# Performance work log

Hardware: AMD Instinct MI355X
Metric: run time of the kernel (lower is better)

The kernel has to match this reference:

```python
import jax, jax.numpy as jnp
import numpy as np

B, N, E, H = 16, 1024, 128, 8  # batch, num_patches, emb_dim, num_heads
INNER = E * H                   # inner_dim = emb_dim * num_heads = 1024
LN_EPS = 1e-5
NEG_MAX = jnp.finfo(jnp.float32).max  # module uses -finfo.max on the diagonal


def setup_inputs() -> dict:
    key = jax.random.key(0)
    k0, k1, k2 = jax.random.split(key, 3)
    x = jax.random.normal(k0, (B, N, E), dtype=jnp.float32)
    ln_w = jnp.ones((E,), jnp.float32)
    ln_b = jnp.zeros((E,), jnp.float32)
    w_qkv = jax.random.normal(k1, (E, 3 * INNER), jnp.float32) * (E ** -0.5)
    scale = jnp.full((H,), E ** -0.5, jnp.float32)  # learnable per-head LSA scale
    w_proj = jax.random.normal(k2, (INNER, E), jnp.float32) * (INNER ** -0.5)
    b_proj = jnp.zeros((E,), jnp.float32)
    return {"x": x, "ln_w": ln_w, "ln_b": ln_b, "w_qkv": w_qkv,
            "scale": scale, "w_proj": w_proj, "b_proj": b_proj}


def reference(x, ln_w, ln_b, w_qkv, scale, w_proj, b_proj):
    # LayerNorm over emb_dim
    mu = jnp.mean(x, axis=-1, keepdims=True)
    var = jnp.mean(jnp.square(x - mu), axis=-1, keepdims=True)
    xn = (x - mu) * jax.lax.rsqrt(var + LN_EPS) * ln_w + ln_b

    # QKV projection (no bias), chunk into q,k,v of [B,N,INNER]
    qkv = xn @ w_qkv
    q, k, v = jnp.split(qkv, 3, axis=-1)

    # 'b n (h d) -> b h n d' with h = H, d = E
    def to_heads(t):
        return t.reshape(B, N, H, E).transpose(0, 2, 1, 3)
    q, k, v = to_heads(q), to_heads(k), to_heads(v)

    # per-head learnable scale (LSA), then mask diagonal to -max
    dots = jnp.einsum("bhnd,bhmd->bhnm", q, k) * scale[None, :, None, None]
    idx = jnp.arange(N)
    dots = dots.at[:, :, idx, idx].set(-NEG_MAX)

    attn = jax.nn.softmax(dots, axis=-1)  # dropout p=0.0 -> identity
    out = jnp.einsum("bhnm,bhmd->bhnd", attn, v)

    # 'b h n d -> b n (h d)', then output projection (with bias)
    out = out.transpose(0, 2, 1, 3).reshape(B, N, INNER)
    return out @ w_proj + b_proj
```

## Files before the change

### kernel.cpp

```cpp
#include <hip/hip_runtime.h>
#include <hip/hip_bf16.h>

typedef __bf16 bf16x8 __attribute__((ext_vector_type(8)));
typedef _Float16 f16x4 __attribute__((ext_vector_type(4)));
typedef float f32x4 __attribute__((ext_vector_type(4)));

__device__ __forceinline__ unsigned short f2bf(float f) {
  union { __hip_bfloat16 h; unsigned short u; } cv;
  cv.h = __float2bfloat16(f);
  return cv.u;
}
__device__ __forceinline__ unsigned short f2h(float f) {
  union { _Float16 h; unsigned short u; } cv;
  cv.h = (_Float16)f;
  return cv.u;
}

__device__ __forceinline__ bf16x8 ld_frag(const unsigned short* p) {
  bf16x8 v;
  __builtin_memcpy(&v, __builtin_assume_aligned(p, 16), 16);
  return v;
}
__device__ __forceinline__ f16x4 ld_h4(const unsigned short* p) {
  f16x4 v;
  __builtin_memcpy(&v, __builtin_assume_aligned(p, 8), 8);
  return v;
}
__device__ __forceinline__ uint4 ld16(const unsigned short* p) {
  uint4 v;
  __builtin_memcpy(&v, __builtin_assume_aligned(p, 16), 16);
  return v;
}
__device__ __forceinline__ void st16(unsigned short* p, uint4 v) {
  __builtin_memcpy(__builtin_assume_aligned(p, 16), &v, 16);
}
__device__ __forceinline__ void dma16(const unsigned short* g, unsigned short* l) {
  __builtin_amdgcn_global_load_lds((const __attribute__((address_space(1))) void*)g,
                                   (__attribute__((address_space(3))) void*)l, 16, 0, 0);
}

__global__ __launch_bounds__(256) void ln_kernel(const float* __restrict__ x,
                                                 const float* __restrict__ w,
                                                 const float* __restrict__ b,
                                                 unsigned short* __restrict__ xn) {
  int wave = threadIdx.x >> 6;
  int lane = threadIdx.x & 63;
  int row = blockIdx.x * 4 + wave;
  const float* xr = x + (size_t)row * 128;
  float2 v = *reinterpret_cast<const float2*>(xr + lane * 2);
  float s1 = v.x + v.y;
  float s2 = v.x * v.x + v.y * v.y;
#pragma unroll
  for (int off = 32; off > 0; off >>= 1) {
    s1 += __shfl_xor(s1, off, 64);
    s2 += __shfl_xor(s2, off, 64);
  }
  float mu = s1 * (1.0f / 128.0f);
  float var = s2 * (1.0f / 128.0f) - mu * mu;
  float rstd = rsqrtf(var + 1e-5f);
  float a0 = (v.x - mu) * rstd * w[lane * 2] + b[lane * 2];
  float a1 = (v.y - mu) * rstd * w[lane * 2 + 1] + b[lane * 2 + 1];
  unsigned int pk = (unsigned int)f2bf(a0) | ((unsigned int)f2bf(a1) << 16);
  *reinterpret_cast<unsigned int*>(xn + (size_t)row * 128 + lane * 2) = pk;
}

__global__ __launch_bounds__(256) void tcast_kernel(const float* __restrict__ in,
                                                    unsigned short* __restrict__ out,
                                                    int R, int C) {
  __shared__ float tile[32][33];
  int tx = threadIdx.x & 31, ty = threadIdx.x >> 5;
  int c0 = blockIdx.x * 32, r0 = blockIdx.y * 32;
#pragma unroll
  for (int k = 0; k < 4; k++)
    tile[ty + 8 * k][tx] = in[(size_t)(r0 + ty + 8 * k) * C + c0 + tx];
  __syncthreads();
#pragma unroll
  for (int k = 0; k < 4; k++)
    out[(size_t)(c0 + ty + 8 * k) * R + r0 + tx] = f2bf(tile[tx][ty + 8 * k]);
}

__global__ __launch_bounds__(256) void qkv_gemm(const unsigned short* __restrict__ A,
                                                const unsigned short* __restrict__ Bt,
                                                const float* __restrict__ scale,
                                                unsigned short* __restrict__ qk,
                                                unsigned short* __restrict__ Vt) {
  __shared__ unsigned short Al[128 * 72];
  __shared__ unsigned short Bl[128 * 72];
  int t = threadIdx.x;
  int i0 = blockIdx.x * 128, c0 = blockIdx.y * 128;
  int lg = t & 7, rr = t >> 3;
  int w = t >> 6, lane = t & 63, l15 = lane & 15, quad = lane >> 4;
  int wy = (w >> 1) * 64, wx = (w & 1) * 64;
  const f32x4 fz = {0.f, 0.f, 0.f, 0.f};
  f32x4 acc[4][4];
#pragma unroll
  for (int i = 0; i < 4; i++)
#pragma unroll
    for (int j = 0; j < 4; j++) acc[i][j] = fz;

#pragma unroll
  for (int kt = 0; kt < 2; kt++) {
    int k0 = kt * 64;
    uint4 areg[4], breg[4];
#pragma unroll
    for (int p = 0; p < 4; p++)
      areg[p] = ld16(&A[(size_t)(i0 + rr + 32 * p) * 128 + k0 + lg * 8]);
#pragma unroll
    for (int p = 0; p < 4; p++)
      breg[p] = ld16(&Bt[(size_t)(c0 + rr + 32 * p) * 128 + k0 + lg * 8]);
    __syncthreads();
#pragma unroll
    for (int p = 0; p < 4; p++) st16(&Al[(rr + 32 * p) * 72 + lg * 8], areg[p]);
#pragma unroll
    for (int p = 0; p < 4; p++) st16(&Bl[(rr + 32 * p) * 72 + lg * 8], breg[p]);
    __syncthreads();
#pragma unroll
    for (int ks = 0; ks < 2; ks++) {
      bf16x8 af[4], bfr[4];
#pragma unroll
      for (int i = 0; i < 4; i++)
        af[i] = ld_frag(&Al[(wy + 16 * i + l15) * 72 + 32 * ks + quad * 8]);
#pragma unroll
      for (int j = 0; j < 4; j++)
        bfr[j] = ld_frag(&Bl[(wx + 16 * j + l15) * 72 + 32 * ks + quad * 8]);
#pragma unroll
      for (int i = 0; i < 4; i++)
#pragma unroll
        for (int j = 0; j < 4; j++)
          acc[i][j] = __builtin_amdgcn_mfma_f32_16x16x32_bf16(af[i], bfr[j], acc[i][j], 0, 0, 0);
    }
  }
  if (blockIdx.y < 16) {
    float qsc = (blockIdx.y < 8) ? scale[blockIdx.y] : 1.0f;
#pragma unroll
    for (int i = 0; i < 4; i++)
#pragma unroll
      for (int j = 0; j < 4; j++)
#pragma unroll
        for (int r = 0; r < 4; r++) {
          int row = i0 + wy + 16 * i + quad * 4 + r;
          int col = c0 + wx + 16 * j + l15;
          qk[(size_t)row * 2048 + col] = f2bf(acc[i][j][r] * qsc);
        }
  } else {
    int vc0 = (blockIdx.y - 16) * 128;
#pragma unroll
    for (int i = 0; i < 4; i++)
#pragma unroll
      for (int j = 0; j < 4; j++) {
        int vcol = vc0 + wx + 16 * j + l15;
        int hh = vcol >> 7, dd = vcol & 127;
        int row0 = i0 + wy + 16 * i + quad * 4;
        int bb = row0 >> 10, nn = row0 & 1023;
        ushort4 pk;
        pk.x = f2h(acc[i][j][0]); pk.y = f2h(acc[i][j][1]);
        pk.z = f2h(acc[i][j][2]); pk.w = f2h(acc[i][j][3]);
        *reinterpret_cast<ushort4*>(Vt + (size_t)(bb * 8 + hh) * 131072 +
                                    (size_t)dd * 1024 + nn) = pk;
      }
  }
}

__global__ __launch_bounds__(256, 3) void attn_kernel(const unsigned short* __restrict__ qk,
                                                      const unsigned short* __restrict__ Vt,
                                                      unsigned short* __restrict__ aout) {
  __shared__ __align__(16) unsigned short Kl[2][64 * 128];
  __shared__ __align__(16) unsigned short Vl[128 * 64];
  int t = threadIdx.x;
  int idx = blockIdx.x;
  int bh = idx & 127, qt = idx >> 7;
  int b = bh >> 3, h = bh & 7;
  int q0 = qt * 128;
  int w = t >> 6, lane = t & 63, l15 = lane & 15, quad = lane >> 4;

  bf16x8 qf[2][4];
  {
    const unsigned short* qb = qk + (size_t)(b * 1024) * 2048 + h * 128;
#pragma unroll
    for (int g = 0; g < 2; g++) {
      const unsigned short* qp = qb + (size_t)(q0 + 32 * w + 16 * g + l15) * 2048;
#pragma unroll
      for (int ks = 0; ks < 4; ks++) qf[g][ks] = ld_frag(qp + 32 * ks + quad * 8);
    }
  }
  const f32x4 fz = {0.f, 0.f, 0.f, 0.f};
  f32x4 o[2][8];
#pragma unroll
  for (int g = 0; g < 2; g++)
#pragma unroll
    for (int i = 0; i < 8; i++) o[g][i] = fz;
  float plsum[2] = {0.f, 0.f};

  const unsigned short* kbase = qk + (size_t)(b * 1024) * 2048 + 1024 + h * 128;
  const unsigned short* vbase = Vt + (size_t)bh * 131072;

  int koff[4], voff[4];
#pragma unroll
  for (int i = 0; i < 4; i++) {
    int c = w * 4 + i;
    int krow = c * 4 + (lane >> 4);
    int kg = ((lane & 15) ^ (krow & 7)) * 8;
    koff[i] = krow * 2048 + kg;
    int vrow = c * 8 + (lane >> 3);
    int vg = ((lane & 7) ^ ((vrow >> 1) & 7)) * 8;
    voff[i] = vrow * 1024 + vg;
  }

#pragma unroll
  for (int i = 0; i < 4; i++) dma16(kbase + koff[i], &Kl[0][(w * 4 + i) * 512]);

  for (int kt = 0; kt < 16; kt++) {
    int k0 = kt * 64;
    __syncthreads();
    {
      int kn0 = ((kt + 1) & 15) * 64;
#pragma unroll
      for (int i = 0; i < 4; i++) dma16(vbase + voff[i] + k0, &Vl[(w * 4 + i) * 512]);
#pragma unroll
      for (int i = 0; i < 4; i++)
        dma16(kbase + (size_t)kn0 * 2048 + koff[i], &Kl[(kt + 1) & 1][(w * 4 + i) * 512]);
    }
    const unsigned short* Kc = Kl[kt & 1];

    f16x4 pa[2][4];
#pragma unroll
    for (int ct = 0; ct < 4; ct++) {
      f32x4 acc[2] = {fz, fz};
#pragma unroll
      for (int ks = 0; ks < 4; ks++) {
        bf16x8 kf = ld_frag(&Kc[(16 * ct + l15) * 128 + ((4 * ks + quad) ^ (l15 & 7)) * 8]);
#pragma unroll
        for (int g = 0; g < 2; g++)
          acc[g] = __builtin_amdgcn_mfma_f32_16x16x32_bf16(kf, qf[g][ks], acc[g], 0, 0, 0);
      }
#pragma unroll
      for (int g = 0; g < 2; g++) {
        if ((q0 + 32 * w + 16 * g) == (k0 + 16 * ct)) {
#pragma unroll
          for (int r = 0; r < 4; r++) {
            float p = ((quad * 4 + r) == l15) ? 0.f : __expf(acc[g][r]);
            plsum[g] += p;
            pa[g][ct][r] = (_Float16)p;
          }
        } else {
#pragma unroll
          for (int r = 0; r < 4; r++) {
            float p = __expf(acc[g][r]);
            plsum[g] += p;
            pa[g][ct][r] = (_Float16)p;
          }
        }
      }
    }

    __syncthreads();

#pragma unroll
    for (int ct = 0; ct < 4; ct++) {
#pragma unroll
      for (int c8 = 0; c8 < 8; c8++) {
        f16x4 vf = ld_h4(&Vl[(16 * c8 + l15) * 64 + ((4 * ct + quad) ^ (l15 & 14)) * 4]);
#pragma unroll
        for (int g = 0; g < 2; g++)
          o[g][c8] = __builtin_amdgcn_mfma_f32_16x16x16f16(pa[g][ct], vf, o[g][c8], 0, 0, 0);
      }
    }
  }

#pragma unroll
  for (int g = 0; g < 2; g++) {
    float s = plsum[g];
    s += __shfl_xor(s, 16, 64);
    s += __shfl_xor(s, 32, 64);
#pragma unroll
    for (int r = 0; r < 4; r++) {
      float rs = __shfl(s, (lane & 48) + quad * 4 + r, 64);
      float rl = 1.0f / rs;
      int row = b * 1024 + q0 + 32 * w + 16 * g + quad * 4 + r;
#pragma unroll
      for (int c8 = 0; c8 < 8; c8++) {
        int col = h * 128 + 16 * c8 + l15;
        aout[(size_t)row * 1024 + col] = f2bf(o[g][c8][r] * rl);
      }
    }
  }
}

__global__ __launch_bounds__(256) void proj_gemm(const unsigned short* __restrict__ A,
                                                 const unsigned short* __restrict__ Bt,
                                                 const float* __restrict__ bias,
                                                 float* __restrict__ out) {
  __shared__ unsigned short Al[64 * 136];
  __shared__ unsigned short Bl[64 * 136];
  int t = threadIdx.x;
  int i0 = blockIdx.x * 64, c0 = blockIdx.y * 64;
  int w = t >> 6, lane = t & 63, l15 = lane & 15, quad = lane >> 4;
  int wy = (w >> 1) * 32, wx = (w & 1) * 32;
  const f32x4 fz = {0.f, 0.f, 0.f, 0.f};
  f32x4 acc[2][2];
#pragma unroll
  for (int i = 0; i < 2; i++)
#pragma unroll
    for (int j = 0; j < 2; j++) acc[i][j] = fz;
  int l = t & 15, rr = t >> 4;
  for (int kb = 0; kb < 8; kb++) {
    int k0 = kb * 128;
    uint4 areg[4], breg[4];
#pragma unroll
    for (int p = 0; p < 4; p++)
      areg[p] = ld16(&A[(size_t)(i0 + rr + 16 * p) * 1024 + k0 + l * 8]);
#pragma unroll
    for (int p = 0; p < 4; p++)
      breg[p] = ld16(&Bt[(size_t)(c0 + rr + 16 * p) * 1024 + k0 + l * 8]);
    __syncthreads();
#pragma unroll
    for (int p = 0; p < 4; p++) st16(&Al[(rr + 16 * p) * 136 + l * 8], areg[p]);
#pragma unroll
    for (int p = 0; p < 4; p++) st16(&Bl[(rr + 16 * p) * 136 + l * 8], breg[p]);
    __syncthreads();
#pragma unroll
    for (int ks = 0; ks < 4; ks++) {
      bf16x8 af[2], bfr[2];
#pragma unroll
      for (int i = 0; i < 2; i++)
        af[i] = ld_frag(&Al[(wy + 16 * i + l15) * 136 + 32 * ks + quad * 8]);
#pragma unroll
      for (int j = 0; j < 2; j++)
        bfr[j] = ld_frag(&Bl[(wx + 16 * j + l15) * 136 + 32 * ks + quad * 8]);
#pragma unroll
      for (int i = 0; i < 2; i++)
#pragma unroll
        for (int j = 0; j < 2; j++)
          acc[i][j] = __builtin_amdgcn_mfma_f32_16x16x32_bf16(af[i], bfr[j], acc[i][j], 0, 0, 0);
    }
  }
#pragma unroll
  for (int i = 0; i < 2; i++)
#pragma unroll
    for (int j = 0; j < 2; j++) {
      int col = c0 + wx + 16 * j + l15;
      float bv = bias[col];
#pragma unroll
      for (int r = 0; r < 4; r++) {
        int row = i0 + wy + 16 * i + quad * 4 + r;
        out[(size_t)row * 128 + col] = acc[i][j][r] + bv;
      }
    }
}

extern "C" void kernel_launch(void* const* d_in, const int* in_sizes, int n_in,
                              void* d_out, int out_size, void* d_ws, size_t ws_size,
                              hipStream_t stream) {
  const float* x      = (const float*)d_in[0];
  const float* ln_w   = (const float*)d_in[1];
  const float* ln_b   = (const float*)d_in[2];
  const float* w_qkv  = (const float*)d_in[3];
  const float* scale  = (const float*)d_in[4];
  const float* w_proj = (const float*)d_in[5];
  const float* b_proj = (const float*)d_in[6];
  float* out = (float*)d_out;

  char* ws = (char*)d_ws;
  unsigned short* xn     = (unsigned short*)(ws);
  unsigned short* wqkvT  = (unsigned short*)(ws + 4194304);
  unsigned short* wprojT = (unsigned short*)(ws + 4980736);
  unsigned short* qk     = (unsigned short*)(ws + 5242880);
  unsigned short* Vt     = (unsigned short*)(ws + 72351744);
  unsigned short* aout   = (unsigned short*)(ws + 105906176);

  ln_kernel<<<dim3(4096), dim3(256), 0, stream>>>(x, ln_w, ln_b, xn);
  tcast_kernel<<<dim3(96, 4), dim3(256), 0, stream>>>(w_qkv, wqkvT, 128, 3072);
  tcast_kernel<<<dim3(4, 32), dim3(256), 0, stream>>>(w_proj, wprojT, 1024, 128);
  qkv_gemm<<<dim3(128, 24), dim3(256), 0, stream>>>(xn, wqkvT, scale, qk, Vt);
  attn_kernel<<<dim3(1024), dim3(256), 0, stream>>>(qk, Vt, aout);
  proj_gemm<<<dim3(256, 2), dim3(256), 0, stream>>>(aout, wprojT, b_proj, out);
}
```

Baseline: 208.2 us.

## Use 16x16x32 f16 MFMA for PV with permuted V layout

Replaces the 16x16x16 f16 MFMA in the P·V product with the double-K 16x16x32 f16 MFMA. Two score tiles are packed into one 8-wide fragment using packed round-toward-zero conversion. The V^T store in the projection kernel now permutes the sequence index so each lane's 8 f16 values line up with the MFMA operand order, which allows 16-byte LDS reads with a new swizzle. This halves the PV MFMA instruction count and LDS load count, at the cost of a more complex layout coupling between the two kernels.

```diff
diff --git a/kernel.cpp b/kernel.cpp
--- a/kernel.cpp
+++ b/kernel.cpp
@@ -2,7 +2,7 @@
 #include <hip/hip_bf16.h>
 
 typedef __bf16 bf16x8 __attribute__((ext_vector_type(8)));
-typedef _Float16 f16x4 __attribute__((ext_vector_type(4)));
+typedef _Float16 f16x8 __attribute__((ext_vector_type(8)));
 typedef float f32x4 __attribute__((ext_vector_type(4)));
 
 __device__ __forceinline__ unsigned short f2bf(float f) {
@@ -15,15 +15,21 @@
   cv.h = (_Float16)f;
   return cv.u;
 }
+__device__ __forceinline__ unsigned int pkrtz(float a, float b) {
+  auto h = __builtin_amdgcn_cvt_pkrtz(a, b);
+  unsigned int u;
+  __builtin_memcpy(&u, &h, 4);
+  return u;
+}
 
 __device__ __forceinline__ bf16x8 ld_frag(const unsigned short* p) {
   bf16x8 v;
   __builtin_memcpy(&v, __builtin_assume_aligned(p, 16), 16);
   return v;
 }
-__device__ __forceinline__ f16x4 ld_h4(const unsigned short* p) {
-  f16x4 v;
-  __builtin_memcpy(&v, __builtin_assume_aligned(p, 8), 8);
+__device__ __forceinline__ f16x8 ld_f16x8(const unsigned short* p) {
+  f16x8 v;
+  __builtin_memcpy(&v, __builtin_assume_aligned(p, 16), 16);
   return v;
 }
 __device__ __forceinline__ uint4 ld16(const unsigned short* p) {
@@ -152,11 +158,12 @@
         int hh = vcol >> 7, dd = vcol & 127;
         int row0 = i0 + wy + 16 * i + quad * 4;
         int bb = row0 >> 10, nn = row0 & 1023;
+        int nnp = (nn & ~31) | (((nn >> 2) & 3) << 3) | (((nn >> 4) & 1) << 2) | (nn & 3);
         ushort4 pk;
         pk.x = f2h(acc[i][j][0]); pk.y = f2h(acc[i][j][1]);
         pk.z = f2h(acc[i][j][2]); pk.w = f2h(acc[i][j][3]);
         *reinterpret_cast<ushort4*>(Vt + (size_t)(bb * 8 + hh) * 131072 +
-                                    (size_t)dd * 1024 + nn) = pk;
+                                    (size_t)dd * 1024 + nnp) = pk;
       }
   }
 }
@@ -222,49 +229,52 @@
     }
     const unsigned short* Kc = Kl[kt & 1];
 
-    f16x4 pa[2][4];
-#pragma unroll
-    for (int ct = 0; ct < 4; ct++) {
-      f32x4 acc[2] = {fz, fz};
-#pragma unroll
-      for (int ks = 0; ks < 4; ks++) {
-        bf16x8 kf = ld_frag(&Kc[(16 * ct + l15) * 128 + ((4 * ks + quad) ^ (l15 & 7)) * 8]);
+    f16x8 pa[2][2];
+#pragma unroll
+    for (int cp = 0; cp < 2; cp++) {
+      unsigned int dw[2][4];
+#pragma unroll
+      for (int sub = 0; sub < 2; sub++) {
+        int ct = cp * 2 + sub;
+        f32x4 acc[2] = {fz, fz};
+#pragma unroll
+        for (int ks = 0; ks < 4; ks++) {
+          bf16x8 kf = ld_frag(&Kc[(16 * ct + l15) * 128 + ((4 * ks + quad) ^ (l15 & 7)) * 8]);
+#pragma unroll
+          for (int g = 0; g < 2; g++)
+            acc[g] = __builtin_amdgcn_mfma_f32_16x16x32_bf16(kf, qf[g][ks], acc[g], 0, 0, 0);
+        }
+#pragma unroll
+        for (int g = 0; g < 2; g++) {
+          float p[4];
+          if ((q0 + 32 * w + 16 * g) == (k0 + 16 * ct)) {
+#pragma unroll
+            for (int r = 0; r < 4; r++)
+              p[r] = ((quad * 4 + r) == l15) ? 0.f : __expf(acc[g][r]);
+          } else {
+#pragma unroll
+            for (int r = 0; r < 4; r++) p[r] = __expf(acc[g][r]);
+          }
+          plsum[g] += (p[0] + p[1]) + (p[2] + p[3]);
+          dw[g][sub * 2 + 0] = pkrtz(p[0], p[1]);
+          dw[g][sub * 2 + 1] = pkrtz(p[2], p[3]);
+        }
+      }
+#pragma unroll
+      for (int g = 0; g < 2; g++) __builtin_memcpy(&pa[g][cp], dw[g], 16);
+    }
+
+    __syncthreads();
+
+#pragma unroll
+    for (int cp = 0; cp < 2; cp++)
+#pragma unroll
+      for (int c8 = 0; c8 < 8; c8++) {
+        f16x8 vf = ld_f16x8(&Vl[(16 * c8 + l15) * 64 + ((4 * cp + quad) ^ ((l15 >> 1) & 7)) * 8]);
 #pragma unroll
         for (int g = 0; g < 2; g++)
-          acc[g] = __builtin_amdgcn_mfma_f32_16x16x32_bf16(kf, qf[g][ks], acc[g], 0, 0, 0);
-      }
-#pragma unroll
-      for (int g = 0; g < 2; g++) {
-        if ((q0 + 32 * w + 16 * g) == (k0 + 16 * ct)) {
-#pragma unroll
-          for (int r = 0; r < 4; r++) {
-            float p = ((quad * 4 + r) == l15) ? 0.f : __expf(acc[g][r]);
-            plsum[g] += p;
-            pa[g][ct][r] = (_Float16)p;
-          }
-        } else {
-#pragma unroll
-          for (int r = 0; r < 4; r++) {
-            float p = __expf(acc[g][r]);
-            plsum[g] += p;
-            pa[g][ct][r] = (_Float16)p;
-          }
-        }
-      }
-    }
-
-    __syncthreads();
-
-#pragma unroll
-    for (int ct = 0; ct < 4; ct++) {
-#pragma unroll
-      for (int c8 = 0; c8 < 8; c8++) {
-        f16x4 vf = ld_h4(&Vl[(16 * c8 + l15) * 64 + ((4 * ct + quad) ^ (l15 & 14)) * 4]);
-#pragma unroll
-        for (int g = 0; g < 2; g++)
-          o[g][c8] = __builtin_amdgcn_mfma_f32_16x16x16f16(pa[g][ct], vf, o[g][c8], 0, 0, 0);
-      }
-    }
+          o[g][c8] = __builtin_amdgcn_mfma_f32_16x16x32_f16(pa[g][cp], vf, o[g][c8], 0, 0, 0);
+      }
   }
 
 #pragma unroll
```

Measured after the change: 194.8 us. 6.4% less time.
